# Optimization experiments

Measured on AMD Instinct MI355X. Metric: run time of the kernel, lower is better.

The kernel has to match this reference:

```python
import jax, jax.numpy as jnp
import numpy as np
from jax import lax

EPS = 1e-5

def conv2d(x, w, b, pad):
    y = lax.conv_general_dilated(x, w, (1, 1), [(pad, pad), (pad, pad)],
                                 dimension_numbers=('NCHW', 'OIHW', 'NCHW'))
    return y + b[None, :, None, None]

def batchnorm(x, gamma, beta):
    mean = jnp.mean(x, axis=(0, 2, 3), keepdims=True)
    var = jnp.var(x, axis=(0, 2, 3), keepdims=True)  # biased, as torch BN training mode
    return gamma[None, :, None, None] * (x - mean) * lax.rsqrt(var + EPS) + beta[None, :, None, None]

def maxpool2(x):
    return lax.reduce_window(x, -jnp.inf, lax.max, (1, 1, 2, 2), (1, 1, 2, 2), 'VALID')

def upsample(x, s):
    N, C, H, W = x.shape
    return jax.image.resize(x, (N, C, H * s, W * s), method='bilinear')

def select_topvar(x, k=3):
    # per-sample, per-channel unbiased variance; gather top-k variance channels
    N, C, H, W = x.shape
    v = jnp.var(x.reshape(N, C, H * W), axis=-1, ddof=1)  # [N, C]
    _, idx = lax.top_k(v, k)                              # argsort(-v)[:k]
    return jnp.take_along_axis(x, idx[:, :, None, None], axis=1)

def setup_inputs() -> dict:
    key = jax.random.key(0)
    ks = jax.random.split(key, 16)
    n_channel, n_class = 10, 5
    d = {}
    d['x'] = jax.random.normal(ks[0], (16, n_channel, 512, 512), jnp.float32)
    sc = 0.1
    d['w_ext1'] = jax.random.normal(ks[1], (16, n_channel, 1, 1), jnp.float32) * sc
    d['b_ext1'] = jnp.zeros((16,), jnp.float32)
    d['g_ebn1'] = jnp.ones((16,), jnp.float32)
    d['be_ebn1'] = jnp.zeros((16,), jnp.float32)
    d['w_ext2'] = jax.random.normal(ks[2], (16, 16, 1, 1), jnp.float32) * sc
    d['b_ext2'] = jnp.zeros((16,), jnp.float32)
    d['g_ebn2'] = jnp.ones((16,), jnp.float32)
    d['be_ebn2'] = jnp.zeros((16,), jnp.float32)
    d['w_c1'] = jax.random.normal(ks[3], (8, 3, 3, 3), jnp.float32) * sc
    d['b_c1'] = jnp.zeros((8,), jnp.float32)
    d['w_c2'] = jax.random.normal(ks[4], (16, 8, 3, 3), jnp.float32) * sc
    d['b_c2'] = jnp.zeros((16,), jnp.float32)
    d['g_bn1'] = jnp.ones((16,), jnp.float32)
    d['be_bn1'] = jnp.zeros((16,), jnp.float32)
    d['g_bn2'] = jnp.ones((8,), jnp.float32)
    d['be_bn2'] = jnp.zeros((8,), jnp.float32)
    d['w_1k'] = jax.random.normal(ks[5], (n_class, 24, 1, 1), jnp.float32) * sc
    d['b_1k'] = jnp.zeros((n_class,), jnp.float32)
    return d

def reference(x, w_ext1, b_ext1, g_ebn1, be_ebn1, w_ext2, b_ext2, g_ebn2, be_ebn2,
              w_c1, b_c1, w_c2, b_c2, g_bn1, be_bn1, g_bn2, be_bn2, w_1k, b_1k):
    # bandExtract: 1x1 conv -> BN -> sigmoid, twice
    h = jax.nn.sigmoid(batchnorm(conv2d(x, w_ext1, b_ext1, 0), g_ebn1, be_ebn1))
    h = jax.nn.sigmoid(batchnorm(conv2d(h, w_ext2, b_ext2, 0), g_ebn2, be_ebn2))
    # featureSelect: keep 3 channels with largest per-sample variance
    x0 = select_topvar(h, 3)                                   # [N,3,H,W]
    x1 = maxpool2(jax.nn.sigmoid(conv2d(x0, w_c1, b_c1, 1)))   # [N,8,H/2,W/2]
    x2 = maxpool2(jax.nn.sigmoid(conv2d(x1, w_c2, b_c2, 1)))   # [N,16,H/4,W/4]
    x2 = batchnorm(jax.nn.relu(upsample(x2, 4)), g_bn1, be_bn1)  # [N,16,H,W]
    x1 = batchnorm(jax.nn.relu(upsample(x1, 2)), g_bn2, be_bn2)  # [N,8,H,W]
    merge = jnp.concatenate([x1, x2], axis=1)                    # [N,24,H,W]
    return conv2d(merge, w_1k, b_1k, 0)                          # [N,n_class,H,W]
```

## Files before the change

kernel.cpp:

```cpp
#include <hip/hip_runtime.h>
#include <math.h>

#define N_    16
#define CIN_  10
#define CB_   16
#define H_    512
#define W_    512
#define HW_   (512*512)
#define EPSF  1e-5f

__device__ __forceinline__ float sgm(float z){
  float e = __builtin_amdgcn_exp2f(z * -1.44269504088896f);
  return __builtin_amdgcn_rcpf(1.0f + e);
}

__global__ void k_zero(double* __restrict__ p, int n){
  int i = blockIdx.x*256 + threadIdx.x;
  if (i < n) p[i] = 0.0;
}

__global__ void k_fin(const double* __restrict__ S, const float* __restrict__ g,
                      const float* __restrict__ be, float* __restrict__ AB,
                      int C, double invM){
  int c = threadIdx.x;
  if (c < C){
    double s=0.0,q=0.0;
    for (int n=0;n<N_;++n){ s+=S[(n*C+c)*2]; q+=S[(n*C+c)*2+1]; }
    double mean = s*invM;
    double var  = q*invM - mean*mean;
    float a = g[c]*rsqrtf((float)var + EPSF);
    AB[c]   = a;
    AB[C+c] = be[c] - (float)mean*a;
  }
}

__global__ __launch_bounds__(256) void k_cov(
    const float* __restrict__ x, double* __restrict__ SP)
{
  const int n = blockIdx.y;
  const int base = blockIdx.x*4096;
  const float* xp = x + (size_t)n*CIN_*HW_;
  float s[CIN_], p[55];
#pragma unroll
  for (int i=0;i<CIN_;++i) s[i]=0.f;
#pragma unroll
  for (int i=0;i<55;++i) p[i]=0.f;
#pragma unroll 1
  for (int it=0; it<4; ++it){
    const int off = base + it*1024 + threadIdx.x*4;
    float4 xv[CIN_];
#pragma unroll
    for (int ci=0; ci<CIN_; ++ci)
      xv[ci] = *(const float4*)(xp + (size_t)ci*HW_ + off);
#pragma unroll
    for (int ci=0; ci<CIN_; ++ci)
      s[ci] += xv[ci].x + xv[ci].y + xv[ci].z + xv[ci].w;
    int k=0;
#pragma unroll
    for (int i=0;i<CIN_;++i)
#pragma unroll
      for (int j=i;j<CIN_;++j,++k)
        p[k] += xv[i].x*xv[j].x + xv[i].y*xv[j].y + xv[i].z*xv[j].z + xv[i].w*xv[j].w;
  }
  __shared__ float red[4][65];
  const int lane = threadIdx.x & 63, wid = threadIdx.x >> 6;
#pragma unroll
  for (int k=0;k<65;++k){
    float v = (k<CIN_) ? s[k] : p[k-CIN_];
    for (int o=32;o>0;o>>=1) v += __shfl_down(v,o);
    if (lane==0) red[wid][k]=v;
  }
  __syncthreads();
  if (threadIdx.x < 65){
    float v = red[0][threadIdx.x]+red[1][threadIdx.x]+red[2][threadIdx.x]+red[3][threadIdx.x];
    atomicAdd(&SP[n*65+threadIdx.x], (double)v);
  }
}

__global__ void k_fin1(const double* __restrict__ SP, const float* __restrict__ w1,
                       const float* __restrict__ b1, const float* __restrict__ g,
                       const float* __restrict__ be, float* __restrict__ AB){
  __shared__ double Sm[CIN_], Cv[55];
  int t = threadIdx.x;
  if (t < 65){
    double s = 0.0;
    for (int n=0;n<N_;++n) s += SP[n*65+t];
    if (t < CIN_) Sm[t] = s; else Cv[t-CIN_] = s;
  }
  __syncthreads();
  if (t < CB_){
    const double M = 16.0*(double)HW_;
    double b = (double)b1[t];
    double wd[CIN_];
    double lin = 0.0;
    for (int i=0;i<CIN_;++i){ wd[i] = (double)w1[t*CIN_+i]; lin += wd[i]*Sm[i]/M; }
    double mean = b + lin;
    double ey2 = b*b + 2.0*b*lin;
    int k=0;
    for (int i=0;i<CIN_;++i)
      for (int j=i;j<CIN_;++j,++k)
        ey2 += (i==j ? 1.0 : 2.0) * wd[i]*wd[j]*(Cv[k]/M);
    double var = ey2 - mean*mean;
    float a = g[t]*rsqrtf((float)var + EPSF);
    AB[t] = a;
    AB[CB_+t] = be[t] - (float)mean*a;
  }
}

__global__ __launch_bounds__(256) void k_band2(
    const float* __restrict__ x,
    const float* __restrict__ w1, const float* __restrict__ b1, const float* __restrict__ AB1,
    const float* __restrict__ w2, const float* __restrict__ b2,
    float* __restrict__ B, double* __restrict__ S2)
{
  const int n = blockIdx.y;
  const int base = blockIdx.x*1024;
  const float* xp = x + (size_t)n*CIN_*HW_;
  float* bp = B + (size_t)n*CB_*HW_;
  float sum[CB_], sq[CB_];
#pragma unroll
  for (int c=0;c<CB_;++c){ sum[c]=0.f; sq[c]=0.f; }
#pragma unroll 1
  for (int it=0; it<4; ++it){
    const int p = base + it*256 + threadIdx.x;
    float xv[CIN_];
#pragma unroll
    for (int ci=0; ci<CIN_; ++ci)
      xv[ci] = xp[(size_t)ci*HW_ + p];
    float s[CB_];
#pragma unroll
    for (int co=0; co<CB_; ++co){
      float o = b1[co];
#pragma unroll
      for (int ci=0; ci<CIN_; ++ci)
        o += w1[co*CIN_+ci]*xv[ci];
      s[co] = sgm(AB1[co]*o + AB1[CB_+co]);
    }
#pragma unroll
    for (int co=0; co<CB_; ++co){
      float o = b2[co];
#pragma unroll
      for (int ci=0; ci<CB_; ++ci)
        o += w2[co*CB_+ci]*s[ci];
      bp[(size_t)co*HW_ + p] = o;
      sum[co] += o;
      sq[co]  += o*o;
    }
  }
  __shared__ float red[4][CB_][2];
  const int lane = threadIdx.x & 63, wid = threadIdx.x >> 6;
#pragma unroll
  for (int c=0;c<CB_;++c){
    float s=sum[c], q=sq[c];
    for (int off=32; off>0; off>>=1){ s += __shfl_down(s,off); q += __shfl_down(q,off); }
    if (lane==0){ red[wid][c][0]=s; red[wid][c][1]=q; }
  }
  __syncthreads();
  if (threadIdx.x < CB_*2){
    int c = threadIdx.x>>1, k = threadIdx.x&1;
    float t = red[0][c][k]+red[1][c][k]+red[2][c][k]+red[3][c][k];
    atomicAdd(&S2[(n*CB_+c)*2+k], (double)t);
  }
}

__global__ __launch_bounds__(256) void k_varstats(
    const float* __restrict__ B, const float* __restrict__ AB2, double* __restrict__ SV)
{
  const int n = blockIdx.z, c = blockIdx.y;
  const float a = AB2[c], b = AB2[CB_+c];
  const float* p = B + ((size_t)(n*CB_+c))*HW_ + blockIdx.x*4096;
  float sum=0.f, sq=0.f;
#pragma unroll 1
  for (int it=0; it<4; ++it){
    float4 v = *(const float4*)(p + it*1024 + threadIdx.x*4);
    v.x = sgm(a*v.x+b); v.y = sgm(a*v.y+b); v.z = sgm(a*v.z+b); v.w = sgm(a*v.w+b);
    sum += v.x+v.y+v.z+v.w;
    sq  += v.x*v.x+v.y*v.y+v.z*v.z+v.w*v.w;
  }
  __shared__ float red[4][2];
  const int lane = threadIdx.x & 63, wid = threadIdx.x >> 6;
  for (int off=32; off>0; off>>=1){ sum += __shfl_down(sum,off); sq += __shfl_down(sq,off); }
  if (lane==0){ red[wid][0]=sum; red[wid][1]=sq; }
  __syncthreads();
  if (threadIdx.x < 2){
    int k = threadIdx.x;
    float t = red[0][k]+red[1][k]+red[2][k]+red[3][k];
    atomicAdd(&SV[(n*CB_+c)*2+k], (double)t);
  }
}

__global__ void k_topk(const double* __restrict__ SV, int* __restrict__ IDX){
  __shared__ double var[N_][CB_];
  int t = threadIdx.x;
  if (t < N_*CB_){
    int n=t>>4, c=t&15;
    double s=SV[t*2], q=SV[t*2+1];
    const double M = (double)HW_;
    var[n][c] = (q - s*s/M)/(M-1.0);
  }
  __syncthreads();
  if (t < N_){
    double v[CB_];
#pragma unroll
    for (int c=0;c<CB_;++c) v[c]=var[t][c];
    for (int k=0;k<3;++k){
      int bi=0; double bv=v[0];
#pragma unroll
      for (int c=1;c<CB_;++c) if (v[c]>bv){ bv=v[c]; bi=c; }
      IDX[t*3+k]=bi; v[bi]=-1e300;
    }
  }
}

__global__ __launch_bounds__(256) void k_conv1p(
    const float* __restrict__ B, const int* __restrict__ IDX, const float* __restrict__ AB2,
    const float* __restrict__ w, const float* __restrict__ bias,
    float* __restrict__ X1)
{
  const int n = blockIdx.y, ho = blockIdx.x, wo = threadIdx.x;
  __shared__ float tile[3][4][516];
  __shared__ int chs[3];
  __shared__ float ca[3], cb[3];
  if (threadIdx.x < 3){
    int c = IDX[n*3+threadIdx.x];
    chs[threadIdx.x] = c;
    ca[threadIdx.x] = AB2[c];
    cb[threadIdx.x] = AB2[CB_+c];
  }
  __syncthreads();
#pragma unroll
  for (int k=0;k<3;++k){
    const float* pc = B + ((size_t)(n*CB_+chs[k]))*HW_;
    const float a = ca[k], bb = cb[k];
#pragma unroll
    for (int dy=0;dy<4;++dy){
      const int r = 2*ho-1+dy;
      float tx = 0.f, ty = 0.f;
      if (r>=0 && r<H_){
        const float2 v = *(const float2*)(pc + (size_t)r*W_ + 2*wo);
        tx = sgm(a*v.x+bb); ty = sgm(a*v.y+bb);
      }
      tile[k][dy][1+2*wo] = tx;
      tile[k][dy][2+2*wo] = ty;
    }
  }
  if (wo < 24){
    int k = wo>>3, dy = (wo&7)>>1;
    tile[k][dy][(wo&1) ? 513 : 0] = 0.f;
  }
  __syncthreads();
  float in[3][4][4];
#pragma unroll
  for (int k=0;k<3;++k)
#pragma unroll
    for (int dy=0;dy<4;++dy)
#pragma unroll
      for (int dx=0;dx<4;++dx)
        in[k][dy][dx] = tile[k][dy][2*wo+dx];
#pragma unroll
  for (int co=0;co<8;++co){
    float m = -1e30f;
#pragma unroll
    for (int py=0;py<2;++py)
#pragma unroll
    for (int px=0;px<2;++px){
      float acc = bias[co];
#pragma unroll
      for (int k=0;k<3;++k)
#pragma unroll
      for (int kh=0;kh<3;++kh)
#pragma unroll
      for (int kw=0;kw<3;++kw)
        acc += w[((co*3+k)*3+kh)*3+kw] * in[k][py+kh][px+kw];
      m = fmaxf(m, acc);
    }
    X1[((size_t)(n*8+co)*256 + ho)*256 + wo] = sgm(m);
  }
}

__global__ __launch_bounds__(256) void k_conv2p(
    const float* __restrict__ X1, const float* __restrict__ w, const float* __restrict__ bias,
    float* __restrict__ X2)
{
  const int n  = blockIdx.y;
  const int wo = threadIdx.x & 127;
  const int ho = blockIdx.x*2 + (threadIdx.x>>7);
  float acc[16][4];
#pragma unroll
  for (int co=0;co<16;++co){
    float bb = bias[co];
    acc[co][0]=bb; acc[co][1]=bb; acc[co][2]=bb; acc[co][3]=bb;
  }
#pragma unroll 1
  for (int ci=0; ci<8; ++ci){
    const float* p = X1 + ((size_t)(n*8+ci))*65536;
    float patch[4][4];
#pragma unroll
    for (int dy=0;dy<4;++dy){
      int r = 2*ho-1+dy;
      bool rok = (r>=0 && r<256);
#pragma unroll
      for (int dx=0;dx<4;++dx){
        int cc = 2*wo-1+dx;
        patch[dy][dx] = (rok && cc>=0 && cc<256) ? p[r*256+cc] : 0.f;
      }
    }
#pragma unroll
    for (int co=0;co<16;++co){
      const float* wp = w + (co*8+ci)*9;
#pragma unroll
      for (int py=0;py<2;++py)
#pragma unroll
      for (int px=0;px<2;++px){
        float a = acc[co][py*2+px];
#pragma unroll
        for (int kh=0;kh<3;++kh)
#pragma unroll
        for (int kw=0;kw<3;++kw)
          a += wp[kh*3+kw]*patch[py+kh][px+kw];
        acc[co][py*2+px] = a;
      }
    }
  }
#pragma unroll
  for (int co=0;co<16;++co){
    float m = fmaxf(fmaxf(acc[co][0],acc[co][1]), fmaxf(acc[co][2],acc[co][3]));
    X2[((size_t)(n*16+co)*128 + ho)*128 + wo] = sgm(m);
  }
}

__global__ __launch_bounds__(256) void k_stats_up4(
    const float* __restrict__ X2, double* __restrict__ SB1)
{
  const int n = blockIdx.z, c = blockIdx.y;
  const float* p = X2 + ((size_t)(n*16+c))*16384;
  const int id = blockIdx.x*256 + threadIdx.x;
  const int ho = id>>7, m = id&127;
  const int q = ho>>2, r = ho&3;
  int rA, rB; float wA;
  if (r==0){ rA=q-1; rB=q;   wA=0.375f; }
  else if (r==1){ rA=q-1; rB=q;   wA=0.125f; }
  else if (r==2){ rA=q;   rB=q+1; wA=0.875f; }
  else          { rA=q;   rB=q+1; wA=0.625f; }
  const float wB = 1.f-wA;
  rA = max(rA,0); rB = min(rB,127);
  const int c0 = max(m-1,0), c1 = m, c2 = min(m+1,127);
  const float* pa = p + rA*128; const float* pb = p + rB*128;
  float t0 = wA*pa[c0]+wB*pb[c0];
  float t1 = wA*pa[c1]+wB*pb[c1];
  float t2 = wA*pa[c2]+wB*pb[c2];
  float o0 = fmaxf(0.375f*t0+0.625f*t1, 0.f);
  float o1 = fmaxf(0.125f*t0+0.875f*t1, 0.f);
  float o2 = fmaxf(0.875f*t1+0.125f*t2, 0.f);
  float o3 = fmaxf(0.625f*t1+0.375f*t2, 0.f);
  float sum = o0+o1+o2+o3;
  float sq  = o0*o0+o1*o1+o2*o2+o3*o3;
  __shared__ float red[4][2];
  const int lane = threadIdx.x & 63, wid = threadIdx.x >> 6;
  for (int off=32; off>0; off>>=1){ sum += __shfl_down(sum,off); sq += __shfl_down(sq,off); }
  if (lane==0){ red[wid][0]=sum; red[wid][1]=sq; }
  __syncthreads();
  if (threadIdx.x < 2){
    int k = threadIdx.x;
    float t = red[0][k]+red[1][k]+red[2][k]+red[3][k];
    atomicAdd(&SB1[(n*16+c)*2+k], (double)t);
  }
}

__global__ __launch_bounds__(256) void k_stats_up2(
    const float* __restrict__ X1, double* __restrict__ SB2)
{
  const int n = blockIdx.z, c = blockIdx.y;
  const float* p = X1 + ((size_t)(n*8+c))*65536;
  const int id = blockIdx.x*256 + threadIdx.x;
  const int ho = id>>7, m = id&127;
  const int i = ho>>1, r = ho&1;
  int rA, rB; float wA;
  if (r==0){ rA=i-1; rB=i;   wA=0.25f; }
  else     { rA=i;   rB=i+1; wA=0.75f; }
  const float wB = 1.f-wA;
  rA = max(rA,0); rB = min(rB,255);
  const int c0 = max(2*m-1,0), c1 = 2*m, c2 = 2*m+1, c3 = min(2*m+2,255);
  const float* pa = p + rA*256; const float* pb = p + rB*256;
  float t0 = wA*pa[c0]+wB*pb[c0];
  float t1 = wA*pa[c1]+wB*pb[c1];
  float t2 = wA*pa[c2]+wB*pb[c2];
  float t3 = wA*pa[c3]+wB*pb[c3];
  float o0 = fmaxf(0.25f*t0+0.75f*t1, 0.f);
  float o1 = fmaxf(0.75f*t1+0.25f*t2, 0.f);
  float o2 = fmaxf(0.25f*t1+0.75f*t2, 0.f);
  float o3 = fmaxf(0.75f*t2+0.25f*t3, 0.f);
  float sum = o0+o1+o2+o3;
  float sq  = o0*o0+o1*o1+o2*o2+o3*o3;
  __shared__ float red[4][2];
  const int lane = threadIdx.x & 63, wid = threadIdx.x >> 6;
  for (int off=32; off>0; off>>=1){ sum += __shfl_down(sum,off); sq += __shfl_down(sq,off); }
  if (lane==0){ red[wid][0]=sum; red[wid][1]=sq; }
  __syncthreads();
  if (threadIdx.x < 2){
    int k = threadIdx.x;
    float t = red[0][k]+red[1][k]+red[2][k]+red[3][k];
    atomicAdd(&SB2[(n*8+c)*2+k], (double)t);
  }
}

__global__ __launch_bounds__(256) void k_final(
    const float* __restrict__ X1, const float* __restrict__ X2,
    const float* __restrict__ ABB1, const float* __restrict__ ABB2,
    const float* __restrict__ w1k, const float* __restrict__ b1k,
    float* __restrict__ out)
{
  const int n = blockIdx.y;
  const int id = blockIdx.x*256 + threadIdx.x;
  const int h = id>>7, m = id&127;
  float acc[5][4];
#pragma unroll
  for (int cls=0;cls<5;++cls){
    float bb = b1k[cls];
    acc[cls][0]=bb; acc[cls][1]=bb; acc[cls][2]=bb; acc[cls][3]=bb;
  }
  {
    const int i = h>>1, r = h&1;
    int rA,rB; float wA;
    if (r==0){ rA=i-1; rB=i;   wA=0.25f; } else { rA=i; rB=i+1; wA=0.75f; }
    const float wB = 1.f-wA;
    rA = max(rA,0); rB = min(rB,255);
    const int c0 = max(2*m-1,0), c1 = 2*m, c2 = 2*m+1, c3 = min(2*m+2,255);
#pragma unroll
    for (int c=0;c<8;++c){
      const float* p  = X1 + ((size_t)(n*8+c))*65536;
      const float* pa = p + rA*256; const float* pb = p + rB*256;
      float t0 = wA*pa[c0]+wB*pb[c0];
      float t1 = wA*pa[c1]+wB*pb[c1];
      float t2 = wA*pa[c2]+wB*pb[c2];
      float t3 = wA*pa[c3]+wB*pb[c3];
      float o0 = 0.25f*t0+0.75f*t1, o1 = 0.75f*t1+0.25f*t2;
      float o2 = 0.25f*t1+0.75f*t2, o3 = 0.75f*t2+0.25f*t3;
      const float a = ABB2[c], bb = ABB2[8+c];
      o0 = a*fmaxf(o0,0.f)+bb; o1 = a*fmaxf(o1,0.f)+bb;
      o2 = a*fmaxf(o2,0.f)+bb; o3 = a*fmaxf(o3,0.f)+bb;
#pragma unroll
      for (int cls=0;cls<5;++cls){
        float wv = w1k[cls*24+c];
        acc[cls][0]+=wv*o0; acc[cls][1]+=wv*o1; acc[cls][2]+=wv*o2; acc[cls][3]+=wv*o3;
      }
    }
  }
  {
    const int q = h>>2, r = h&3;
    int rA,rB; float wA;
    if (r==0){ rA=q-1; rB=q;   wA=0.375f; }
    else if (r==1){ rA=q-1; rB=q;   wA=0.125f; }
    else if (r==2){ rA=q;   rB=q+1; wA=0.875f; }
    else          { rA=q;   rB=q+1; wA=0.625f; }
    const float wB = 1.f-wA;
    rA = max(rA,0); rB = min(rB,127);
    const int c0 = max(m-1,0), c1 = m, c2 = min(m+1,127);
#pragma unroll
    for (int c=0;c<16;++c){
      const float* p  = X2 + ((size_t)(n*16+c))*16384;
      const float* pa = p + rA*128; const float* pb = p + rB*128;
      float t0 = wA*pa[c0]+wB*pb[c0];
      float t1 = wA*pa[c1]+wB*pb[c1];
      float t2 = wA*pa[c2]+wB*pb[c2];
      float o0 = 0.375f*t0+0.625f*t1;
      float o1 = 0.125f*t0+0.875f*t1;
      float o2 = 0.875f*t1+0.125f*t2;
      float o3 = 0.625f*t1+0.375f*t2;
      const float a = ABB1[c], bb = ABB1[16+c];
      o0 = a*fmaxf(o0,0.f)+bb; o1 = a*fmaxf(o1,0.f)+bb;
      o2 = a*fmaxf(o2,0.f)+bb; o3 = a*fmaxf(o3,0.f)+bb;
#pragma unroll
      for (int cls=0;cls<5;++cls){
        float wv = w1k[cls*24+8+c];
        acc[cls][0]+=wv*o0; acc[cls][1]+=wv*o1; acc[cls][2]+=wv*o2; acc[cls][3]+=wv*o3;
      }
    }
  }
#pragma unroll
  for (int cls=0;cls<5;++cls){
    float4 v; v.x=acc[cls][0]; v.y=acc[cls][1]; v.z=acc[cls][2]; v.w=acc[cls][3];
    *(float4*)(out + ((size_t)(n*5+cls))*HW_ + (size_t)h*W_ + 4*m) = v;
  }
}

extern "C" void kernel_launch(void* const* d_in, const int* in_sizes, int n_in,
                              void* d_out, int out_size, void* d_ws, size_t ws_size,
                              hipStream_t stream) {
  const float* x       = (const float*)d_in[0];
  const float* w_ext1  = (const float*)d_in[1];
  const float* b_ext1  = (const float*)d_in[2];
  const float* g_ebn1  = (const float*)d_in[3];
  const float* be_ebn1 = (const float*)d_in[4];
  const float* w_ext2  = (const float*)d_in[5];
  const float* b_ext2  = (const float*)d_in[6];
  const float* g_ebn2  = (const float*)d_in[7];
  const float* be_ebn2 = (const float*)d_in[8];
  const float* w_c1    = (const float*)d_in[9];
  const float* b_c1    = (const float*)d_in[10];
  const float* w_c2    = (const float*)d_in[11];
  const float* b_c2    = (const float*)d_in[12];
  const float* g_bn1   = (const float*)d_in[13];
  const float* be_bn1  = (const float*)d_in[14];
  const float* g_bn2   = (const float*)d_in[15];
  const float* be_bn2  = (const float*)d_in[16];
  const float* w_1k    = (const float*)d_in[17];
  const float* b_1k    = (const float*)d_in[18];
  float* outp = (float*)d_out;

  char* ws = (char*)d_ws;
  float* B  = (float*)ws;
  float* X1 = (float*)(ws + 268435456);
  float* X2 = (float*)(ws + 268435456 + 33554432);
  char*  sb = ws + 268435456 + 33554432 + 16777216;
  double* SP  = (double*)sb;
  double* S2  = SP  + 1040;
  double* SV  = S2  + 512;
  double* SB1 = SV  + 512;
  double* SB2 = SB1 + 512;
  float*  AB1  = (float*)(SB2 + 256);
  float*  AB2  = AB1 + 32;
  float*  ABB1 = AB2 + 32;
  float*  ABB2 = ABB1 + 32;
  int*    IDX  = (int*)(ABB2 + 16);

  const double invM_bn = 1.0/4194304.0;

  k_zero<<<12,256,0,stream>>>(SP, 2832);
  k_cov<<<dim3(64,16),256,0,stream>>>(x, SP);
  k_fin1<<<1,128,0,stream>>>(SP, w_ext1, b_ext1, g_ebn1, be_ebn1, AB1);
  k_band2<<<dim3(256,16),256,0,stream>>>(x, w_ext1, b_ext1, AB1, w_ext2, b_ext2, B, S2);
  k_fin<<<1,64,0,stream>>>(S2, g_ebn2, be_ebn2, AB2, 16, invM_bn);
  k_varstats<<<dim3(64,16,16),256,0,stream>>>(B, AB2, SV);
  k_topk<<<1,256,0,stream>>>(SV, IDX);
  k_conv1p<<<dim3(256,16),256,0,stream>>>(B, IDX, AB2, w_c1, b_c1, X1);
  k_conv2p<<<dim3(64,16),256,0,stream>>>(X1, w_c2, b_c2, X2);
  k_stats_up4<<<dim3(256,16,16),256,0,stream>>>(X2, SB1);
  k_stats_up2<<<dim3(256,8,16),256,0,stream>>>(X1, SB2);
  k_fin<<<1,64,0,stream>>>(SB1, g_bn1, be_bn1, ABB1, 16, invM_bn);
  k_fin<<<1,64,0,stream>>>(SB2, g_bn2, be_bn2, ABB2, 8, invM_bn);
  k_final<<<dim3(256,16),256,0,stream>>>(X1, X2, ABB1, ABB2, w_1k, b_1k, outp);
}
```

Before: 800.1 us.

## Recompute band features from input instead of materializing 16-channel intermediate

Removes the full 16-channel intermediate buffer. The stats pass, the variance pass and the selected-channel pass each recompute the two 1x1 conv+sigmoid stages from the input. Only the 3 top-variance channels are written, already activated, so conv1 no longer applies BN and sigmoid. This trades large global writes and reads for reading the input three times and repeating the per-pixel matmul work.

```diff
diff --git a/kernel.cpp b/kernel.cpp
--- a/kernel.cpp
+++ b/kernel.cpp
@@ -107,16 +107,15 @@
   }
 }
 
-__global__ __launch_bounds__(256) void k_band2(
+__global__ __launch_bounds__(256) void k_s2(
     const float* __restrict__ x,
     const float* __restrict__ w1, const float* __restrict__ b1, const float* __restrict__ AB1,
     const float* __restrict__ w2, const float* __restrict__ b2,
-    float* __restrict__ B, double* __restrict__ S2)
+    double* __restrict__ S2)
 {
   const int n = blockIdx.y;
   const int base = blockIdx.x*1024;
   const float* xp = x + (size_t)n*CIN_*HW_;
-  float* bp = B + (size_t)n*CB_*HW_;
   float sum[CB_], sq[CB_];
 #pragma unroll
   for (int c=0;c<CB_;++c){ sum[c]=0.f; sq[c]=0.f; }
@@ -142,7 +141,6 @@
 #pragma unroll
       for (int ci=0; ci<CB_; ++ci)
         o += w2[co*CB_+ci]*s[ci];
-      bp[(size_t)co*HW_ + p] = o;
       sum[co] += o;
       sq[co]  += o*o;
     }
@@ -163,28 +161,57 @@
   }
 }
 
-__global__ __launch_bounds__(256) void k_varstats(
-    const float* __restrict__ B, const float* __restrict__ AB2, double* __restrict__ SV)
-{
-  const int n = blockIdx.z, c = blockIdx.y;
-  const float a = AB2[c], b = AB2[CB_+c];
-  const float* p = B + ((size_t)(n*CB_+c))*HW_ + blockIdx.x*4096;
-  float sum=0.f, sq=0.f;
+__global__ __launch_bounds__(256) void k_sv(
+    const float* __restrict__ x,
+    const float* __restrict__ w1, const float* __restrict__ b1, const float* __restrict__ AB1,
+    const float* __restrict__ w2, const float* __restrict__ b2, const float* __restrict__ AB2,
+    double* __restrict__ SV)
+{
+  const int n = blockIdx.y;
+  const int base = blockIdx.x*1024;
+  const float* xp = x + (size_t)n*CIN_*HW_;
+  float sum[CB_], sq[CB_];
+#pragma unroll
+  for (int c=0;c<CB_;++c){ sum[c]=0.f; sq[c]=0.f; }
 #pragma unroll 1
   for (int it=0; it<4; ++it){
-    float4 v = *(const float4*)(p + it*1024 + threadIdx.x*4);
-    v.x = sgm(a*v.x+b); v.y = sgm(a*v.y+b); v.z = sgm(a*v.z+b); v.w = sgm(a*v.w+b);
-    sum += v.x+v.y+v.z+v.w;
-    sq  += v.x*v.x+v.y*v.y+v.z*v.z+v.w*v.w;
-  }
-  __shared__ float red[4][2];
+    const int p = base + it*256 + threadIdx.x;
+    float xv[CIN_];
+#pragma unroll
+    for (int ci=0; ci<CIN_; ++ci)
+      xv[ci] = xp[(size_t)ci*HW_ + p];
+    float s[CB_];
+#pragma unroll
+    for (int co=0; co<CB_; ++co){
+      float o = b1[co];
+#pragma unroll
+      for (int ci=0; ci<CIN_; ++ci)
+        o += w1[co*CIN_+ci]*xv[ci];
+      s[co] = sgm(AB1[co]*o + AB1[CB_+co]);
+    }
+#pragma unroll
+    for (int co=0; co<CB_; ++co){
+      float o = b2[co];
+#pragma unroll
+      for (int ci=0; ci<CB_; ++ci)
+        o += w2[co*CB_+ci]*s[ci];
+      float h = sgm(AB2[co]*o + AB2[CB_+co]);
+      sum[co] += h;
+      sq[co]  += h*h;
+    }
+  }
+  __shared__ float red[4][CB_][2];
   const int lane = threadIdx.x & 63, wid = threadIdx.x >> 6;
-  for (int off=32; off>0; off>>=1){ sum += __shfl_down(sum,off); sq += __shfl_down(sq,off); }
-  if (lane==0){ red[wid][0]=sum; red[wid][1]=sq; }
-  __syncthreads();
-  if (threadIdx.x < 2){
-    int k = threadIdx.x;
-    float t = red[0][k]+red[1][k]+red[2][k]+red[3][k];
+#pragma unroll
+  for (int c=0;c<CB_;++c){
+    float s=sum[c], q=sq[c];
+    for (int off=32; off>0; off>>=1){ s += __shfl_down(s,off); q += __shfl_down(q,off); }
+    if (lane==0){ red[wid][c][0]=s; red[wid][c][1]=q; }
+  }
+  __syncthreads();
+  if (threadIdx.x < CB_*2){
+    int c = threadIdx.x>>1, k = threadIdx.x&1;
+    float t = red[0][c][k]+red[1][c][k]+red[2][c][k]+red[3][c][k];
     atomicAdd(&SV[(n*CB_+c)*2+k], (double)t);
   }
 }
@@ -212,33 +239,68 @@
   }
 }
 
+__global__ __launch_bounds__(256) void k_b3(
+    const float* __restrict__ x,
+    const float* __restrict__ w1, const float* __restrict__ b1, const float* __restrict__ AB1,
+    const float* __restrict__ w2, const float* __restrict__ b2, const float* __restrict__ AB2,
+    const int* __restrict__ IDX, float* __restrict__ H3)
+{
+  const int n = blockIdx.y;
+  __shared__ float wsel[3][CB_], bsel[3], asel[3], shsel[3];
+  if (threadIdx.x < 48){
+    int k = threadIdx.x >> 4, ci = threadIdx.x & 15;
+    int c = IDX[n*3+k];
+    wsel[k][ci] = w2[c*CB_+ci];
+    if (ci==0){ bsel[k]=b2[c]; asel[k]=AB2[c]; shsel[k]=AB2[CB_+c]; }
+  }
+  __syncthreads();
+  const int base = blockIdx.x*1024;
+  const float* xp = x + (size_t)n*CIN_*HW_;
+  float* hp = H3 + (size_t)n*3*HW_;
+#pragma unroll 1
+  for (int it=0; it<4; ++it){
+    const int p = base + it*256 + threadIdx.x;
+    float xv[CIN_];
+#pragma unroll
+    for (int ci=0; ci<CIN_; ++ci)
+      xv[ci] = xp[(size_t)ci*HW_ + p];
+    float s[CB_];
+#pragma unroll
+    for (int co=0; co<CB_; ++co){
+      float o = b1[co];
+#pragma unroll
+      for (int ci=0; ci<CIN_; ++ci)
+        o += w1[co*CIN_+ci]*xv[ci];
+      s[co] = sgm(AB1[co]*o + AB1[CB_+co]);
+    }
+#pragma unroll
+    for (int k=0;k<3;++k){
+      float o = bsel[k];
+#pragma unroll
+      for (int ci=0; ci<CB_; ++ci)
+        o += wsel[k][ci]*s[ci];
+      hp[(size_t)k*HW_ + p] = sgm(asel[k]*o + shsel[k]);
+    }
+  }
+}
+
 __global__ __launch_bounds__(256) void k_conv1p(
-    const float* __restrict__ B, const int* __restrict__ IDX, const float* __restrict__ AB2,
+    const float* __restrict__ H3,
     const float* __restrict__ w, const float* __restrict__ bias,
     float* __restrict__ X1)
 {
   const int n = blockIdx.y, ho = blockIdx.x, wo = threadIdx.x;
   __shared__ float tile[3][4][516];
-  __shared__ int chs[3];
-  __shared__ float ca[3], cb[3];
-  if (threadIdx.x < 3){
-    int c = IDX[n*3+threadIdx.x];
-    chs[threadIdx.x] = c;
-    ca[threadIdx.x] = AB2[c];
-    cb[threadIdx.x] = AB2[CB_+c];
-  }
-  __syncthreads();
 #pragma unroll
   for (int k=0;k<3;++k){
-    const float* pc = B + ((size_t)(n*CB_+chs[k]))*HW_;
-    const float a = ca[k], bb = cb[k];
+    const float* pc = H3 + ((size_t)(n*3+k))*HW_;
 #pragma unroll
     for (int dy=0;dy<4;++dy){
       const int r = 2*ho-1+dy;
       float tx = 0.f, ty = 0.f;
       if (r>=0 && r<H_){
         const float2 v = *(const float2*)(pc + (size_t)r*W_ + 2*wo);
-        tx = sgm(a*v.x+bb); ty = sgm(a*v.y+bb);
+        tx = v.x; ty = v.y;
       }
       tile[k][dy][1+2*wo] = tx;
       tile[k][dy][2+2*wo] = ty;
@@ -509,7 +571,7 @@
   float* outp = (float*)d_out;
 
   char* ws = (char*)d_ws;
-  float* B  = (float*)ws;
+  float* H3 = (float*)ws;
   float* X1 = (float*)(ws + 268435456);
   float* X2 = (float*)(ws + 268435456 + 33554432);
   char*  sb = ws + 268435456 + 33554432 + 16777216;
@@ -529,11 +591,12 @@
   k_zero<<<12,256,0,stream>>>(SP, 2832);
   k_cov<<<dim3(64,16),256,0,stream>>>(x, SP);
   k_fin1<<<1,128,0,stream>>>(SP, w_ext1, b_ext1, g_ebn1, be_ebn1, AB1);
-  k_band2<<<dim3(256,16),256,0,stream>>>(x, w_ext1, b_ext1, AB1, w_ext2, b_ext2, B, S2);
+  k_s2<<<dim3(256,16),256,0,stream>>>(x, w_ext1, b_ext1, AB1, w_ext2, b_ext2, S2);
   k_fin<<<1,64,0,stream>>>(S2, g_ebn2, be_ebn2, AB2, 16, invM_bn);
-  k_varstats<<<dim3(64,16,16),256,0,stream>>>(B, AB2, SV);
+  k_sv<<<dim3(256,16),256,0,stream>>>(x, w_ext1, b_ext1, AB1, w_ext2, b_ext2, AB2, SV);
   k_topk<<<1,256,0,stream>>>(SV, IDX);
-  k_conv1p<<<dim3(256,16),256,0,stream>>>(B, IDX, AB2, w_c1, b_c1, X1);
+  k_b3<<<dim3(256,16),256,0,stream>>>(x, w_ext1, b_ext1, AB1, w_ext2, b_ext2, AB2, IDX, H3);
+  k_conv1p<<<dim3(256,16),256,0,stream>>>(H3, w_c1, b_c1, X1);
   k_conv2p<<<dim3(64,16),256,0,stream>>>(X1, w_c2, b_c2, X2);
   k_stats_up4<<<dim3(256,16,16),256,0,stream>>>(X2, SB1);
   k_stats_up2<<<dim3(256,8,16),256,0,stream>>>(X1, SB2);
```

Result: slower. 1.044 ms (+30.4%).
